# Optimization experiments

Measured on AMD Instinct MI355X. Metric: run time of the kernel, lower is better.

The kernel has to match this reference:

```python
import jax, jax.numpy as jnp
import numpy as np

B, C, H, W, N = 8, 128, 128, 256, 1024
E1_LAMDA = 1.0
E2_LAMDA = 2.0 / 7.0
EPS = 1e-9


def bilinear_sample(fmap, xs):
    """fmap: (B,C,H,W); xs: (B,N,2) with (x,y) pixel coords -> (B*N, C)."""
    Wd, Hd = fmap.shape[3], fmap.shape[2]
    x = jnp.clip(xs[..., 0], 0.0, Wd - 1.0)
    y = jnp.clip(xs[..., 1], 0.0, Hd - 1.0)
    x0 = jnp.clip(jnp.floor(x).astype(jnp.int32), 0, Wd - 2)
    y0 = jnp.clip(jnp.floor(y).astype(jnp.int32), 0, Hd - 2)
    x1, y1 = x0 + 1, y0 + 1
    wx = (x - x0)[..., None]  # (B,N,1)
    wy = (y - y0)[..., None]
    bidx = jnp.arange(fmap.shape[0])[:, None]  # (B,1) broadcasts with (B,N)
    f00 = fmap[bidx, :, y0, x0]  # (B,N,C)
    f01 = fmap[bidx, :, y0, x1]
    f10 = fmap[bidx, :, y1, x0]
    f11 = fmap[bidx, :, y1, x1]
    out = (f00 * (1 - wx) * (1 - wy) + f01 * wx * (1 - wy)
           + f10 * (1 - wx) * wy + f11 * wx * wy)
    return out.reshape(-1, fmap.shape[1])  # (B*N, C)


def setup_inputs() -> dict:
    key = jax.random.key(0)
    k1, k2, k3, k4 = jax.random.split(key, 4)
    fb = jax.random.normal(k1, (B, C, H, W), dtype=jnp.float32)
    # positive match coords (x in [1,W-2], y in [1,H-2]) so noise stays in-bounds-ish
    ub = jax.random.uniform(k2, (B, N, 2), dtype=jnp.float32) \
         * jnp.array([W - 3.0, H - 3.0], jnp.float32) + 1.0
    noise = jax.random.uniform(k3, (B, N, 2), dtype=jnp.float32, minval=-1.0, maxval=1.0)
    f_t = jax.random.normal(k4, (B * N, C), dtype=jnp.float32)
    return {"fb": fb, "f_t": f_t, "ub": ub, "noise": noise}


def reference(fb, f_t, ub, noise):
    xs = ub + noise                                   # perturbed sample points (B,N,2)
    f_s = bilinear_sample(fb, xs)                     # (BN, C)
    r = f_s - f_t                                     # residual
    # np.gradient-style central differences (one-sided at edges)
    gx = jnp.gradient(fb, axis=3)
    gy = jnp.gradient(fb, axis=2)
    Jx = bilinear_sample(gx, xs)                      # (BN, C)
    Jy = bilinear_sample(gy, xs)
    J = jnp.stack([Jx, Jy], axis=-1)                  # (BN, C, 2)
    Hm = jnp.einsum('nci,ncj->nij', J, J) + EPS * jnp.eye(2, dtype=fb.dtype)
    b = jnp.einsum('nci,nc->ni', J, r)                # (BN, 2)
    # analytic 2x2 inverse
    a_, b_, c_, d_ = Hm[:, 0, 0], Hm[:, 0, 1], Hm[:, 1, 0], Hm[:, 1, 1]
    det = a_ * d_ - b_ * c_
    Hinv = jnp.stack([jnp.stack([d_, -b_], -1),
                      jnp.stack([-c_, a_], -1)], -2) / det[:, None, None]
    miu = xs.reshape(-1, 2) - jnp.einsum('nij,nj->ni', Hinv, b)  # (BN, 2)
    diff = ub.reshape(-1, 2) - miu
    e1 = 0.5 * jnp.sum(jnp.einsum('ni,nij,nj->n', diff, Hm, diff))
    det_c = jnp.clip(det, 1e-16, None)
    e2 = (B * N) * jnp.log(jnp.asarray(2.0 * np.pi, fb.dtype)) - 0.5 * jnp.sum(jnp.log(det_c))
    e = E1_LAMDA * e1 + E2_LAMDA * e2
    return (e, e1, e2)
```

## Files before the change

kernel.cpp:

```cpp
#include <hip/hip_runtime.h>

#define Bq 8
#define Cq 128
#define Hq 128
#define Wq 256
#define Nq 1024
#define BN (Bq * Nq)
#define HWq (Hq * Wq)
#define FBT_ELEMS ((size_t)Bq * Cq * HWq)

#define LOG_2PI 1.8378770664093453f
#define EPSq 1e-9f

__global__ __launch_bounds__(256) void transpose_nchw_nhwc(
    const float* __restrict__ in, float* __restrict__ out)
{
    __shared__ float tile[64][65];
    const int blk = blockIdx.x;
    const int ct = blk & 1;
    const int pt = (blk >> 1) & 511;
    const int b  = blk >> 10;
    const int c0 = ct << 6;
    const int p0 = pt << 6;
    const int tx = threadIdx.x & 63;
    const int ty = threadIdx.x >> 6;

    const float* src = in + ((size_t)b * Cq + c0) * HWq + p0;
    #pragma unroll
    for (int i = 0; i < 16; ++i) {
        const int cy = ty + (i << 2);
        tile[cy][tx] = src[(size_t)cy * HWq + tx];
    }
    __syncthreads();
    float* dst = out + ((size_t)b * HWq + p0) * Cq + c0;
    #pragma unroll
    for (int i = 0; i < 16; ++i) {
        const int py = ty + (i << 2);
        dst[(size_t)py * Cq + tx] = tile[tx][py];
    }
}

__global__ __launch_bounds__(64) void gn_sample_nhwc(
    const float* __restrict__ fbT,
    const float* __restrict__ f_t,
    const float* __restrict__ ub,
    const float* __restrict__ noise,
    float* __restrict__ partials)
{
    const int n = blockIdx.x;
    const int b = n >> 10;
    const int lane = threadIdx.x;

    const float ubx = ub[2 * n];
    const float uby = ub[2 * n + 1];
    const float xsx = ubx + noise[2 * n];
    const float xsy = uby + noise[2 * n + 1];

    float x = fminf(fmaxf(xsx, 0.0f), (float)(Wq - 1));
    float y = fminf(fmaxf(xsy, 0.0f), (float)(Hq - 1));
    int x0 = (int)floorf(x); x0 = min(max(x0, 0), Wq - 2);
    int y0 = (int)floorf(y); y0 = min(max(y0, 0), Hq - 2);
    const int x1 = x0 + 1, y1 = y0 + 1;
    const float wx = x - (float)x0;
    const float wy = y - (float)y0;

    const int xlo0 = max(x0 - 1, 0);
    const int xhi1 = min(x1 + 1, Wq - 1);
    const int ylo0 = max(y0 - 1, 0);
    const int yhi1 = min(y1 + 1, Hq - 1);
    const float sx0 = 1.0f / (float)(x1 - xlo0);
    const float sx1 = 1.0f / (float)(xhi1 - x0);
    const float sy0 = 1.0f / (float)(y1 - ylo0);
    const float sy1 = 1.0f / (float)(yhi1 - y0);

    const size_t bb = (size_t)b * HWq;
    const int co = lane * 2;
    #define PT(yy, xx) (*(const float2*)(fbT + ((bb + (size_t)(yy) * Wq + (xx)) * Cq + co)))

    const float2 f_lo0 = PT(ylo0, x0), f_lo1 = PT(ylo0, x1);
    const float2 f0m = PT(y0, xlo0), f00 = PT(y0, x0), f01 = PT(y0, x1), f0p = PT(y0, xhi1);
    const float2 f1m = PT(y1, xlo0), f10 = PT(y1, x0), f11 = PT(y1, x1), f1p = PT(y1, xhi1);
    const float2 f_hi0 = PT(yhi1, x0), f_hi1 = PT(yhi1, x1);
    #undef PT

    const float2 ft = *(const float2*)(f_t + (size_t)n * Cq + co);

    const float w00 = (1.0f - wx) * (1.0f - wy);
    const float w01 = wx * (1.0f - wy);
    const float w10 = (1.0f - wx) * wy;
    const float w11 = wx * wy;

    float hxx = 0.0f, hxy = 0.0f, hyy = 0.0f, bx = 0.0f, by = 0.0f;
    #pragma unroll
    for (int k = 0; k < 2; ++k) {
        const float vlo0 = (k ? f_lo0.y : f_lo0.x), vlo1 = (k ? f_lo1.y : f_lo1.x);
        const float v0m = (k ? f0m.y : f0m.x), v00 = (k ? f00.y : f00.x);
        const float v01 = (k ? f01.y : f01.x), v0p = (k ? f0p.y : f0p.x);
        const float v1m = (k ? f1m.y : f1m.x), v10 = (k ? f10.y : f10.x);
        const float v11 = (k ? f11.y : f11.x), v1p = (k ? f1p.y : f1p.x);
        const float vhi0 = (k ? f_hi0.y : f_hi0.x), vhi1 = (k ? f_hi1.y : f_hi1.x);
        const float vt = (k ? ft.y : ft.x);

        const float gx00 = (v01 - v0m) * sx0;
        const float gx01 = (v0p - v00) * sx1;
        const float gx10 = (v11 - v1m) * sx0;
        const float gx11 = (v1p - v10) * sx1;
        const float gy00 = (v10 - vlo0) * sy0;
        const float gy01 = (v11 - vlo1) * sy0;
        const float gy10 = (vhi0 - v00) * sy1;
        const float gy11 = (vhi1 - v01) * sy1;

        const float fs = v00 * w00 + v01 * w01 + v10 * w10 + v11 * w11;
        const float Jx = gx00 * w00 + gx01 * w01 + gx10 * w10 + gx11 * w11;
        const float Jy = gy00 * w00 + gy01 * w01 + gy10 * w10 + gy11 * w11;
        const float r  = fs - vt;

        hxx += Jx * Jx;
        hxy += Jx * Jy;
        hyy += Jy * Jy;
        bx  += Jx * r;
        by  += Jy * r;
    }

    #pragma unroll
    for (int off = 32; off > 0; off >>= 1) {
        hxx += __shfl_down(hxx, off);
        hxy += __shfl_down(hxy, off);
        hyy += __shfl_down(hyy, off);
        bx  += __shfl_down(bx, off);
        by  += __shfl_down(by, off);
    }

    if (lane == 0) {
        const float A  = hxx + EPSq;
        const float Bv = hxy;
        const float D  = hyy + EPSq;

        const float det = A * D - Bv * Bv;
        const float inv = 1.0f / det;
        const float hbx = ( D * bx - Bv * by) * inv;
        const float hby = (-Bv * bx + A * by) * inv;
        const float dx = ubx - (xsx - hbx);
        const float dy = uby - (xsy - hby);
        const float quad = A * dx * dx + 2.0f * Bv * dx * dy + D * dy * dy;

        const float detc = fmaxf(det, 1e-16f);
        partials[n]      = 0.5f * quad;
        partials[BN + n] = logf(detc);
    }
}

__global__ __launch_bounds__(1024) void gn_reduce_kernel(
    const float* __restrict__ partials, float* __restrict__ out)
{
    float s1 = 0.0f, s2 = 0.0f;
    for (int i = threadIdx.x; i < BN; i += 1024) {
        s1 += partials[i];
        s2 += partials[BN + i];
    }
    #pragma unroll
    for (int off = 32; off > 0; off >>= 1) {
        s1 += __shfl_down(s1, off);
        s2 += __shfl_down(s2, off);
    }
    __shared__ float l1[16], l2[16];
    const int w = threadIdx.x >> 6;
    if ((threadIdx.x & 63) == 0) { l1[w] = s1; l2[w] = s2; }
    __syncthreads();
    if (threadIdx.x == 0) {
        float e1 = 0.0f, sl = 0.0f;
        #pragma unroll
        for (int i = 0; i < 16; ++i) { e1 += l1[i]; sl += l2[i]; }
        const float e2 = (float)BN * LOG_2PI - 0.5f * sl;
        out[0] = e1 + (2.0f / 7.0f) * e2;
        out[1] = e1;
        out[2] = e2;
    }
}

extern "C" void kernel_launch(void* const* d_in, const int* in_sizes, int n_in,
                              void* d_out, int out_size, void* d_ws, size_t ws_size,
                              hipStream_t stream) {
    const float* fb    = (const float*)d_in[0];
    const float* f_t   = (const float*)d_in[1];
    const float* ub    = (const float*)d_in[2];
    const float* noise = (const float*)d_in[3];
    float* out = (float*)d_out;
    float* wsf = (float*)d_ws;
    float* fbT      = wsf;
    float* partials = wsf + FBT_ELEMS;

    transpose_nchw_nhwc<<<Bq * (HWq / 64) * (Cq / 64), 256, 0, stream>>>(fb, fbT);
    gn_sample_nhwc<<<BN, 64, 0, stream>>>(fbT, f_t, ub, noise, partials);
    gn_reduce_kernel<<<1, 1024, 0, stream>>>(partials, out);
}
```

Before: 233.8 us.

## Vectorize transpose with XOR-swizzled 128x128 tile and pack four points per sample block

The NCHW-to-NHWC transpose now handles a full 128-channel by 128-pixel tile per 512-thread block. It uses float4 global loads and stores, and an XOR swizzle in LDS stands in for the padded tile. The point is wider memory transactions and fewer blocks in what is mainly a bandwidth-bound pass over the whole feature map. The sample kernel now runs four points per 256-thread block (one wavefront each) instead of one point per 64-thread block, which cuts the block count. The 64KB LDS tile limits how many transpose blocks fit on each CU, and the scalar swizzled LDS writes may still cause bank conflicts.

New measurement: 233.7 us. About the same (-0.0%).

```diff
diff --git a/kernel.cpp b/kernel.cpp
--- a/kernel.cpp
+++ b/kernel.cpp
@@ -12,44 +12,51 @@
 #define LOG_2PI 1.8378770664093453f
 #define EPSq 1e-9f
 
-__global__ __launch_bounds__(256) void transpose_nchw_nhwc(
+__global__ __launch_bounds__(512) void transpose_nchw_nhwc(
     const float* __restrict__ in, float* __restrict__ out)
 {
-    __shared__ float tile[64][65];
+    __shared__ float tile[128 * 128];
     const int blk = blockIdx.x;
-    const int ct = blk & 1;
-    const int pt = (blk >> 1) & 511;
-    const int b  = blk >> 10;
-    const int c0 = ct << 6;
-    const int p0 = pt << 6;
-    const int tx = threadIdx.x & 63;
-    const int ty = threadIdx.x >> 6;
-
-    const float* src = in + ((size_t)b * Cq + c0) * HWq + p0;
-    #pragma unroll
-    for (int i = 0; i < 16; ++i) {
-        const int cy = ty + (i << 2);
-        tile[cy][tx] = src[(size_t)cy * HWq + tx];
+    const int pt = blk & 255;
+    const int b  = blk >> 8;
+    const int p0 = pt << 7;
+    const int fx = threadIdx.x & 31;
+    const int cr = threadIdx.x >> 5;
+
+    const float* src = in + (size_t)b * Cq * HWq + p0;
+    #pragma unroll
+    for (int pass = 0; pass < 8; ++pass) {
+        const int c = cr + (pass << 4);
+        const float4 v = *(const float4*)(src + (size_t)c * HWq + 4 * fx);
+        const int c4 = c >> 2, cl = c & 3;
+        #pragma unroll
+        for (int j = 0; j < 4; ++j) {
+            const int p = 4 * fx + j;
+            const float vj = j == 0 ? v.x : (j == 1 ? v.y : (j == 2 ? v.z : v.w));
+            tile[p * 128 + ((c4 ^ (p & 31)) << 2) + cl] = vj;
+        }
     }
     __syncthreads();
-    float* dst = out + ((size_t)b * HWq + p0) * Cq + c0;
-    #pragma unroll
-    for (int i = 0; i < 16; ++i) {
-        const int py = ty + (i << 2);
-        dst[(size_t)py * Cq + tx] = tile[tx][py];
-    }
-}
-
-__global__ __launch_bounds__(64) void gn_sample_nhwc(
+    float* dst = out + ((size_t)b * HWq + p0) * Cq;
+    #pragma unroll
+    for (int pass = 0; pass < 8; ++pass) {
+        const int p = (threadIdx.x >> 5) + (pass << 4);
+        const int c4 = threadIdx.x & 31;
+        const float4 v = *(const float4*)(tile + p * 128 + ((c4 ^ (p & 31)) << 2));
+        *(float4*)(dst + (size_t)p * Cq + 4 * c4) = v;
+    }
+}
+
+__global__ __launch_bounds__(256) void gn_sample_nhwc(
     const float* __restrict__ fbT,
     const float* __restrict__ f_t,
     const float* __restrict__ ub,
     const float* __restrict__ noise,
     float* __restrict__ partials)
 {
-    const int n = blockIdx.x;
+    const int n = (blockIdx.x << 2) + (threadIdx.x >> 6);
     const int b = n >> 10;
-    const int lane = threadIdx.x;
+    const int lane = threadIdx.x & 63;
 
     const float ubx = ub[2 * n];
     const float uby = ub[2 * n + 1];
@@ -190,7 +197,7 @@
     float* fbT      = wsf;
     float* partials = wsf + FBT_ELEMS;
 
-    transpose_nchw_nhwc<<<Bq * (HWq / 64) * (Cq / 64), 256, 0, stream>>>(fb, fbT);
-    gn_sample_nhwc<<<BN, 64, 0, stream>>>(fbT, f_t, ub, noise, partials);
+    transpose_nchw_nhwc<<<Bq * (HWq / 128), 512, 0, stream>>>(fb, fbT);
+    gn_sample_nhwc<<<BN / 4, 256, 0, stream>>>(fbT, f_t, ub, noise, partials);
     gn_reduce_kernel<<<1, 1024, 0, stream>>>(partials, out);
 }
```
